# Performance work log

Measured on AMD Instinct MI355X. Metric: run time of the kernel, lower is better.

## Reference

```python
import jax, jax.numpy as jnp
import numpy as np

N_NODES = 50000
N_EDGES = 800000
IN_CH = 128
HID = 32
HEADS = 8
EMB = 64
NEG_SLOPE = 0.2


def _segment_softmax(e, seg, num_segments):
    # e: [E, H] edge scores, seg: [E] destination node ids
    m = jax.ops.segment_max(e, seg, num_segments=num_segments)
    ex = jnp.exp(e - m[seg])
    denom = jax.ops.segment_sum(ex, seg, num_segments=num_segments)
    return ex / (denom[seg] + 1e-16)


def gat_conv(x, src, dst, W, a_src, a_dst, bias, heads, out_ch):
    # x: [N, F_in]; W: [F_in, heads*out_ch]; a_src/a_dst: [heads, out_ch]; bias: [heads*out_ch]
    n = x.shape[0]
    h = (x @ W).reshape(n, heads, out_ch)                 # [N, H, C]
    alpha_src = jnp.sum(h * a_src[None], axis=-1)         # [N, H]
    alpha_dst = jnp.sum(h * a_dst[None], axis=-1)         # [N, H]
    e = jax.nn.leaky_relu(alpha_src[src] + alpha_dst[dst], NEG_SLOPE)  # [E, H]
    alpha = _segment_softmax(e, dst, n)                   # [E, H]
    msg = h[src] * alpha[:, :, None]                      # [E, H, C]
    out = jax.ops.segment_sum(msg, dst, num_segments=n)   # [N, H, C]
    return out.reshape(n, heads * out_ch) + bias


def _with_self_loops(edge_index, n):
    # PyG GATConv default add_self_loops=True
    loop = jnp.arange(n, dtype=edge_index.dtype)
    src = jnp.concatenate([edge_index[0], loop])
    dst = jnp.concatenate([edge_index[1], loop])
    return src, dst


def setup_inputs() -> dict:
    key = jax.random.key(0)
    ks = jax.random.split(key, 16)
    x = jax.random.normal(ks[0], (N_NODES, IN_CH), dtype=jnp.float32)
    edge_index = jax.random.randint(ks[1], (2, N_EDGES), 0, N_NODES, dtype=jnp.int32)

    def glorot(k, shape):
        fan = sum(shape[-2:]) if len(shape) >= 2 else shape[-1]
        return jax.random.normal(k, shape, dtype=jnp.float32) * jnp.sqrt(2.0 / fan)

    # conv1: IN_CH -> HID x HEADS (concat)
    W1 = glorot(ks[2], (IN_CH, HEADS * HID))
    a_src1 = glorot(ks[3], (HEADS, HID))
    a_dst1 = glorot(ks[4], (HEADS, HID))
    b1 = jnp.zeros((HEADS * HID,), jnp.float32)
    # conv2: HID*HEADS -> HID, heads=1
    W2 = glorot(ks[5], (HEADS * HID, HID))
    a_src2 = glorot(ks[6], (1, HID))
    a_dst2 = glorot(ks[7], (1, HID))
    b2 = jnp.zeros((HID,), jnp.float32)
    # conv3: HID -> EMB, heads=1
    W3 = glorot(ks[8], (HID, EMB))
    a_src3 = glorot(ks[9], (1, EMB))
    a_dst3 = glorot(ks[10], (1, EMB))
    b3 = jnp.zeros((EMB,), jnp.float32)
    return {"x": x, "edge_index": edge_index,
            "W1": W1, "a_src1": a_src1, "a_dst1": a_dst1, "b1": b1,
            "W2": W2, "a_src2": a_src2, "a_dst2": a_dst2, "b2": b2,
            "W3": W3, "a_src3": a_src3, "a_dst3": a_dst3, "b3": b3}


def reference(x, edge_index, W1, a_src1, a_dst1, b1, W2, a_src2, a_dst2, b2,
              W3, a_src3, a_dst3, b3):
    src, dst = _with_self_loops(edge_index, x.shape[0])
    h = gat_conv(x, src, dst, W1, a_src1, a_dst1, b1, HEADS, HID)
    h = jax.nn.elu(h)  # dropout is identity in eval mode
    h = gat_conv(h, src, dst, W2, a_src2, a_dst2, b2, 1, HID)
    h = jax.nn.elu(h)
    out = gat_conv(h, src, dst, W3, a_src3, a_dst3, b3, 1, EMB)
    return out
```

## Files before the change

### kernel.cpp

```cpp
#include <hip/hip_runtime.h>
#include <hip/hip_bf16.h>
#include <math.h>

#define N_NODES 50000
#define N_EDGES 800000
#define ET (N_EDGES + N_NODES)
#define F0 128
#define H1 8
#define C1 32
#define D1 (H1*C1)
#define C2 32
#define C3 64
#define CAP 128

typedef unsigned short u16;
typedef unsigned int u32;
typedef __attribute__((ext_vector_type(8))) short short8;
typedef __attribute__((ext_vector_type(4))) float f32x4;

__device__ __forceinline__ float lrelu(float x) { return x >= 0.f ? x : 0.2f * x; }
__device__ __forceinline__ float eluf(float x)  { return x > 0.f ? x : (expf(x) - 1.f); }

__device__ __forceinline__ u16 f2bf(float f) {
    u32 u = __float_as_uint(f);
    return (u16)((u + 0x7FFFu + ((u >> 16) & 1u)) >> 16);
}
__device__ __forceinline__ u32 pack2bf(float lo, float hi) {
    return ((u32)f2bf(hi) << 16) | (u32)f2bf(lo);
}
__device__ __forceinline__ float bf2f(u16 v) {
    return __uint_as_float((u32)v << 16);
}
__device__ __forceinline__ float4 bf4_to_f4(uint2 v) {
    float4 r;
    r.x = __uint_as_float(v.x << 16);
    r.y = __uint_as_float(v.x & 0xFFFF0000u);
    r.z = __uint_as_float(v.y << 16);
    r.w = __uint_as_float(v.y & 0xFFFF0000u);
    return r;
}


__global__ void prep_kernel(const float* __restrict__ W1, const float* __restrict__ W2,
                            const float* __restrict__ W3,
                            u16* __restrict__ W1t, u16* __restrict__ W2t, u16* __restrict__ W3t,
                            int* __restrict__ cnt) {
    int t = blockIdx.x * 256 + threadIdx.x;
    if (t < N_NODES) cnt[t] = 0;
    if (t < F0 * D1) {
        int n = t >> 7, k = t & 127;
        W1t[n * F0 + k] = f2bf(W1[(size_t)k * D1 + n]);
    }
    if (t < D1 * C2) {
        int k = t >> 5, n = t & 31;
        W2t[n * D1 + k] = f2bf(W2[t]);
    }
    if (t < C2 * C3) {
        int k = t >> 6, n = t & 63;
        W3t[n * C2 + k] = f2bf(W3[t]);
    }
}


__global__ void scatterF_kernel(const int* __restrict__ srcArr, const int* __restrict__ dstArr,
                                int* __restrict__ cnt, int* __restrict__ csrF) {
    int e = blockIdx.x * 256 + threadIdx.x;
    if (e >= ET) return;
    int s, d;
    if (e < N_EDGES) { s = srcArr[e]; d = dstArr[e]; } else { s = d = e - N_EDGES; }
    int pos = atomicAdd(&cnt[d], 1);
    csrF[d * CAP + pos] = s;
}


#define WKS 136

__global__ __launch_bounds__(512, 2) void gemm1_mfma(const u16* __restrict__ W1t,
                                                     const float* __restrict__ x,
                                                     const float* __restrict__ aS1,
                                                     const float* __restrict__ aD1,
                                                     u16* __restrict__ h1b,
                                                     float* __restrict__ as,
                                                     float* __restrict__ ad, int M) {
    __shared__ u16 Wt[128][WKS];
    int tid = threadIdx.x;
    int bm = blockIdx.x * 128;

    int w = tid >> 6, lane = tid & 63, l15 = lane & 15, q = lane >> 4;
    int mr = bm + w * 16 + l15;
    if (mr > M - 1) mr = M - 1;

    short8 af[4];
#pragma unroll
    for (int kc = 0; kc < 4; ++kc) {
        const float* ap = x + (size_t)mr * F0 + kc * 32 + q * 8;
        float4 a0 = *(const float4*)ap;
        float4 a1 = *(const float4*)(ap + 4);
        af[kc][0] = (short)f2bf(a0.x); af[kc][1] = (short)f2bf(a0.y);
        af[kc][2] = (short)f2bf(a0.z); af[kc][3] = (short)f2bf(a0.w);
        af[kc][4] = (short)f2bf(a1.x); af[kc][5] = (short)f2bf(a1.y);
        af[kc][6] = (short)f2bf(a1.z); af[kc][7] = (short)f2bf(a1.w);
    }

    f32x4 acc[16];
#pragma unroll
    for (int t = 0; t < 16; ++t) acc[t] = (f32x4){0.f, 0.f, 0.f, 0.f};

#pragma unroll
    for (int half = 0; half < 2; ++half) {
        __syncthreads();
        for (int idx = tid; idx < 128 * F0 / 8; idx += 512) {
            int n = idx >> 4, c = idx & 15;
            *(short8*)&Wt[n][c * 8] =
                *(const short8*)(W1t + (size_t)(half * 128 + n) * F0 + c * 8);
        }
        __syncthreads();
#pragma unroll
        for (int t = 0; t < 8; ++t) {
#pragma unroll
            for (int kc = 0; kc < 4; ++kc) {
                short8 bf = *(const short8*)&Wt[t * 16 + l15][kc * 32 + q * 8];
                acc[half * 8 + t] =
                    __builtin_amdgcn_mfma_f32_16x16x32_bf16(af[kc], bf, acc[half * 8 + t], 0, 0, 0);
            }
        }
    }

#pragma unroll
    for (int r = 0; r < 4; ++r) {
        int row = bm + w * 16 + q * 4 + r;
        if (row >= M) continue;
        size_t base = (size_t)row * D1;
#pragma unroll
        for (int t = 0; t < 16; ++t)
            h1b[base + t * 16 + l15] = f2bf(acc[t][r]);
    }

#pragma unroll
    for (int lh = 0; lh < 8; ++lh) {
        float aS0  = aS1[lh * 32 + l15];
        float aS16 = aS1[lh * 32 + 16 + l15];
        float aD0  = aD1[lh * 32 + l15];
        float aD16 = aD1[lh * 32 + 16 + l15];
#pragma unroll
        for (int r = 0; r < 4; ++r) {
            float s1 = acc[2 * lh][r] * aS0 + acc[2 * lh + 1][r] * aS16;
            float s2 = acc[2 * lh][r] * aD0 + acc[2 * lh + 1][r] * aD16;
            s1 += __shfl_xor(s1, 1); s1 += __shfl_xor(s1, 2);
            s1 += __shfl_xor(s1, 4); s1 += __shfl_xor(s1, 8);
            s2 += __shfl_xor(s2, 1); s2 += __shfl_xor(s2, 2);
            s2 += __shfl_xor(s2, 4); s2 += __shfl_xor(s2, 8);
            int row = bm + w * 16 + q * 4 + r;
            if (l15 == 0 && row < M) {
                as[row * 8 + lh] = s1;
                ad[row * 8 + lh] = s2;
            }
        }
    }
}


__global__ __launch_bounds__(256) void gemm2_mfma(const u16* __restrict__ A,
                                                  const u16* __restrict__ W2t,
                                                  const float* __restrict__ aS2,
                                                  const float* __restrict__ aD2,
                                                  u16* __restrict__ h2b,
                                                  float* __restrict__ as,
                                                  float* __restrict__ ad, int M) {
    int tid = threadIdx.x;
    int bm = blockIdx.x * 64;
    int w = tid >> 6, lane = tid & 63, l15 = lane & 15, q = lane >> 4;
    int mr = bm + w * 16 + l15;
    if (mr > M - 1) mr = M - 1;

    f32x4 acc0 = {0.f, 0.f, 0.f, 0.f};
    f32x4 acc1 = {0.f, 0.f, 0.f, 0.f};
    const u16* b0p = W2t + (size_t)(0 * 16 + l15) * D1;
    const u16* b1p = W2t + (size_t)(1 * 16 + l15) * D1;
#pragma unroll
    for (int k0 = 0; k0 < D1; k0 += 32) {
        short8 af = *(const short8*)(A + (size_t)mr * D1 + k0 + q * 8);
        short8 b0 = *(const short8*)(b0p + k0 + q * 8);
        short8 b1 = *(const short8*)(b1p + k0 + q * 8);
        acc0 = __builtin_amdgcn_mfma_f32_16x16x32_bf16(af, b0, acc0, 0, 0, 0);
        acc1 = __builtin_amdgcn_mfma_f32_16x16x32_bf16(af, b1, acc1, 0, 0, 0);
    }

    float aS0 = aS2[l15], aS16 = aS2[16 + l15];
    float aD0 = aD2[l15], aD16 = aD2[16 + l15];
#pragma unroll
    for (int r = 0; r < 4; ++r) {
        int row = bm + w * 16 + q * 4 + r;
        float s1 = acc0[r] * aS0 + acc1[r] * aS16;
        float s2 = acc0[r] * aD0 + acc1[r] * aD16;
        s1 += __shfl_xor(s1, 1); s1 += __shfl_xor(s1, 2);
        s1 += __shfl_xor(s1, 4); s1 += __shfl_xor(s1, 8);
        s2 += __shfl_xor(s2, 1); s2 += __shfl_xor(s2, 2);
        s2 += __shfl_xor(s2, 4); s2 += __shfl_xor(s2, 8);
        if (row < M) {
            h2b[(size_t)row * C2 + 0 * 16 + l15] = f2bf(acc0[r]);
            h2b[(size_t)row * C2 + 1 * 16 + l15] = f2bf(acc1[r]);
            if (l15 == 0) { as[row] = s1; ad[row] = s2; }
        }
    }
}


__global__ __launch_bounds__(256) void gemm3_mfma(const u16* __restrict__ A,
                                                  const u16* __restrict__ W3t,
                                                  const float* __restrict__ aS3,
                                                  const float* __restrict__ aD3,
                                                  u16* __restrict__ h3b,
                                                  float* __restrict__ as,
                                                  float* __restrict__ ad, int M) {
    int tid = threadIdx.x;
    int bm = blockIdx.x * 64;
    int w = tid >> 6, lane = tid & 63, l15 = lane & 15, q = lane >> 4;
    int mr = bm + w * 16 + l15;
    if (mr > M - 1) mr = M - 1;

    short8 af = *(const short8*)(A + (size_t)mr * C2 + q * 8);

    f32x4 acc[4];
#pragma unroll
    for (int t = 0; t < 4; ++t) {
        short8 bf = *(const short8*)(W3t + (size_t)(t * 16 + l15) * C2 + q * 8);
        f32x4 z = {0.f, 0.f, 0.f, 0.f};
        acc[t] = __builtin_amdgcn_mfma_f32_16x16x32_bf16(af, bf, z, 0, 0, 0);
    }

    float aSv[4], aDv[4];
#pragma unroll
    for (int t = 0; t < 4; ++t) {
        aSv[t] = aS3[t * 16 + l15];
        aDv[t] = aD3[t * 16 + l15];
    }
#pragma unroll
    for (int r = 0; r < 4; ++r) {
        int row = bm + w * 16 + q * 4 + r;
        float s1 = acc[0][r] * aSv[0] + acc[1][r] * aSv[1] + acc[2][r] * aSv[2] + acc[3][r] * aSv[3];
        float s2 = acc[0][r] * aDv[0] + acc[1][r] * aDv[1] + acc[2][r] * aDv[2] + acc[3][r] * aDv[3];
        s1 += __shfl_xor(s1, 1); s1 += __shfl_xor(s1, 2);
        s1 += __shfl_xor(s1, 4); s1 += __shfl_xor(s1, 8);
        s2 += __shfl_xor(s2, 1); s2 += __shfl_xor(s2, 2);
        s2 += __shfl_xor(s2, 4); s2 += __shfl_xor(s2, 8);
        if (row < M) {
            size_t base = (size_t)row * C3;
#pragma unroll
            for (int t = 0; t < 4; ++t)
                h3b[base + t * 16 + l15] = f2bf(acc[t][r]);
            if (l15 == 0) { as[row] = s1; ad[row] = s2; }
        }
    }
}


__global__ __launch_bounds__(256) void agg1_kernel(const int* __restrict__ cnt, const int* __restrict__ csrF,
                                                   const u16* __restrict__ h, const float* __restrict__ as,
                                                   const float* __restrict__ ad, const float* __restrict__ bias,
                                                   u16* __restrict__ outb) {
    int node = blockIdx.x * 4 + (threadIdx.x >> 6);
    if (node >= N_NODES) return;
    int lane = threadIdx.x & 63;
    int hh = lane >> 3;
    int j  = lane & 7;
    int s0 = node * CAP;
    int deg = cnt[node];
    int dmain = deg < 64 ? deg : 64;
    int idxv = (lane < dmain) ? __builtin_nontemporal_load(csrF + s0 + lane) : 0;
    float adw = ad[node * H1 + j];
    const u16* hb = h + hh * C1 + j * 4;

    float4 acc = make_float4(0.f, 0.f, 0.f, 0.f);
    float wsum = 0.f;
    for (int base = 0; base < dmain; base += 8) {
        int sw = __shfl(idxv, base + hh);
        float myw = 0.f;
        if (base + hh < dmain)
            myw = __expf(lrelu(as[sw * H1 + j] + adw));
        wsum += myw;
        int su[8]; uint2 v[8]; float wu[8];
#pragma unroll
        for (int u = 0; u < 8; ++u) su[u] = __shfl(idxv, base + u);
#pragma unroll
        for (int u = 0; u < 8; ++u) v[u] = *(const uint2*)(hb + (size_t)su[u] * D1);
#pragma unroll
        for (int u = 0; u < 8; ++u) wu[u] = __shfl(myw, u * 8 + hh);
#pragma unroll
        for (int u = 0; u < 8; ++u) {
            float4 hv = bf4_to_f4(v[u]);
            acc.x += wu[u] * hv.x;
            acc.y += wu[u] * hv.y;
            acc.z += wu[u] * hv.z;
            acc.w += wu[u] * hv.w;
        }
    }
    float ws = wsum;
    ws += __shfl_xor(ws, 8);
    ws += __shfl_xor(ws, 16);
    ws += __shfl_xor(ws, 32);
    float dsum = __shfl(ws, hh);

    for (int i = 64; i < deg; ++i) {
        int s = csrF[s0 + i];
        float4 hv = bf4_to_f4(*(const uint2*)(hb + (size_t)s * D1));
        float w = __expf(lrelu(as[s * H1 + hh] + ad[node * H1 + hh]));
        dsum += w;
        acc.x += w * hv.x; acc.y += w * hv.y; acc.z += w * hv.z; acc.w += w * hv.w;
    }

    float inv = 1.f / (dsum + 1e-16f);
    int ob = node * D1 + hh * C1 + j * 4;
    const float* bp = bias + hh * C1 + j * 4;
    float rx = eluf(acc.x * inv + bp[0]);
    float ry = eluf(acc.y * inv + bp[1]);
    float rz = eluf(acc.z * inv + bp[2]);
    float rw = eluf(acc.w * inv + bp[3]);
    uint2 pr;
    pr.x = pack2bf(rx, ry);
    pr.y = pack2bf(rz, rw);
    *(uint2*)(outb + ob) = pr;
}


__global__ __launch_bounds__(256) void agg32_kernel(const int* __restrict__ cnt, const int* __restrict__ csrF,
                                                    const u16* __restrict__ h, const float* __restrict__ as,
                                                    const float* __restrict__ ad, const float* __restrict__ bias,
                                                    u16* __restrict__ outb) {
    int node = blockIdx.x * 4 + (threadIdx.x >> 6);
    if (node >= N_NODES) return;
    int lane = threadIdx.x & 63;
    int eg = lane >> 3;
    int cg = lane & 7;
    int s0 = node * CAP;
    int deg = cnt[node];
    int dmain = deg < 64 ? deg : 64;
    int idxv = (lane < dmain) ? __builtin_nontemporal_load(csrF + s0 + lane) : 0;
    float adv = ad[node];

    float wfull = 0.f;
    if (lane < dmain) wfull = __expf(lrelu(as[idxv] + adv));
    float ws = wfull;
#pragma unroll
    for (int o = 1; o < 64; o <<= 1) ws += __shfl_xor(ws, o);
    float dsum = ws;

    float4 acc = make_float4(0.f, 0.f, 0.f, 0.f);
    for (int base = 0; base < dmain; base += 16) {
        int i0 = base + eg;
        int i1 = i0 + 8;
        int sa = __shfl(idxv, i0);
        int sb = __shfl(idxv, i1);
        float wa = __shfl(wfull, i0);
        float wb = __shfl(wfull, i1);
        uint2 va = *(const uint2*)(h + (size_t)sa * C2 + cg * 4);
        uint2 vb = *(const uint2*)(h + (size_t)sb * C2 + cg * 4);
        float4 ha = bf4_to_f4(va);
        float4 hb = bf4_to_f4(vb);
        acc.x += wa * ha.x + wb * hb.x;
        acc.y += wa * ha.y + wb * hb.y;
        acc.z += wa * ha.z + wb * hb.z;
        acc.w += wa * ha.w + wb * hb.w;
    }
    float extra = 0.f;
    for (int i = 64 + eg; i < deg; i += 8) {
        int s = csrF[s0 + i];
        float4 hv = bf4_to_f4(*(const uint2*)(h + (size_t)s * C2 + cg * 4));
        float w = __expf(lrelu(as[s] + adv));
        extra += w;
        acc.x += w * hv.x; acc.y += w * hv.y; acc.z += w * hv.z; acc.w += w * hv.w;
    }
#pragma unroll
    for (int o = 8; o < 64; o <<= 1) {
        acc.x += __shfl_xor(acc.x, o);
        acc.y += __shfl_xor(acc.y, o);
        acc.z += __shfl_xor(acc.z, o);
        acc.w += __shfl_xor(acc.w, o);
        extra += __shfl_xor(extra, o);
    }
    dsum += extra;
    if (eg == 0) {
        float inv = 1.f / (dsum + 1e-16f);
        const float* bp = bias + cg * 4;
        float rx = eluf(acc.x * inv + bp[0]);
        float ry = eluf(acc.y * inv + bp[1]);
        float rz = eluf(acc.z * inv + bp[2]);
        float rw = eluf(acc.w * inv + bp[3]);
        uint2 pr;
        pr.x = pack2bf(rx, ry);
        pr.y = pack2bf(rz, rw);
        *(uint2*)(outb + (size_t)node * C2 + cg * 4) = pr;
    }
}


__global__ __launch_bounds__(256) void agg64_kernel(const int* __restrict__ cnt, const int* __restrict__ csrF,
                                                    const u16* __restrict__ h, const float* __restrict__ as,
                                                    const float* __restrict__ ad, const float* __restrict__ bias,
                                                    float* __restrict__ out) {
    int node = blockIdx.x * 4 + (threadIdx.x >> 6);
    if (node >= N_NODES) return;
    int lane = threadIdx.x & 63;
    int eg = lane >> 4;
    int cg = lane & 15;
    int s0 = node * CAP;
    int deg = cnt[node];
    int dmain = deg < 64 ? deg : 64;
    int idxv = (lane < dmain) ? __builtin_nontemporal_load(csrF + s0 + lane) : 0;
    float adv = ad[node];

    float wfull = 0.f;
    if (lane < dmain) wfull = __expf(lrelu(as[idxv] + adv));
    float ws = wfull;
#pragma unroll
    for (int o = 1; o < 64; o <<= 1) ws += __shfl_xor(ws, o);
    float dsum = ws;

    float4 acc = make_float4(0.f, 0.f, 0.f, 0.f);
    for (int base = 0; base < dmain; base += 8) {
        int i0 = base + eg;
        int i1 = i0 + 4;
        int sa = __shfl(idxv, i0);
        int sb = __shfl(idxv, i1);
        float wa = __shfl(wfull, i0);
        float wb = __shfl(wfull, i1);
        uint2 va = *(const uint2*)(h + (size_t)sa * C3 + cg * 4);
        uint2 vb = *(const uint2*)(h + (size_t)sb * C3 + cg * 4);
        float4 ha = bf4_to_f4(va);
        float4 hb = bf4_to_f4(vb);
        acc.x += wa * ha.x + wb * hb.x;
        acc.y += wa * ha.y + wb * hb.y;
        acc.z += wa * ha.z + wb * hb.z;
        acc.w += wa * ha.w + wb * hb.w;
    }
    float extra = 0.f;
    for (int i = 64 + eg; i < deg; i += 4) {
        int s = csrF[s0 + i];
        float4 hv = bf4_to_f4(*(const uint2*)(h + (size_t)s * C3 + cg * 4));
        float w = __expf(lrelu(as[s] + adv));
        extra += w;
        acc.x += w * hv.x; acc.y += w * hv.y; acc.z += w * hv.z; acc.w += w * hv.w;
    }
#pragma unroll
    for (int o = 16; o < 64; o <<= 1) {
        acc.x += __shfl_xor(acc.x, o);
        acc.y += __shfl_xor(acc.y, o);
        acc.z += __shfl_xor(acc.z, o);
        acc.w += __shfl_xor(acc.w, o);
        extra += __shfl_xor(extra, o);
    }
    dsum += extra;
    if (eg == 0) {
        float inv = 1.f / (dsum + 1e-16f);
        const float* bp = bias + cg * 4;
        float4 r;
        r.x = acc.x * inv + bp[0];
        r.y = acc.y * inv + bp[1];
        r.z = acc.z * inv + bp[2];
        r.w = acc.w * inv + bp[3];
        *(float4*)(out + (size_t)node * C3 + cg * 4) = r;
    }
}


extern "C" void kernel_launch(void* const* d_in, const int* in_sizes, int n_in,
                              void* d_out, int out_size, void* d_ws, size_t ws_size,
                              hipStream_t stream) {
    const float* x   = (const float*)d_in[0];
    const int*   ei  = (const int*)d_in[1];
    const float* W1  = (const float*)d_in[2];
    const float* aS1 = (const float*)d_in[3];
    const float* aD1 = (const float*)d_in[4];
    const float* b1  = (const float*)d_in[5];
    const float* W2  = (const float*)d_in[6];
    const float* aS2 = (const float*)d_in[7];
    const float* aD2 = (const float*)d_in[8];
    const float* b2  = (const float*)d_in[9];
    const float* W3  = (const float*)d_in[10];
    const float* aS3 = (const float*)d_in[11];
    const float* aD3 = (const float*)d_in[12];
    const float* b3  = (const float*)d_in[13];
    float* out = (float*)d_out;

    char* p = (char*)d_ws;
    auto alloc = [&](size_t bytes) -> void* {
        void* r = (void*)p;
        p += (bytes + 255) & ~(size_t)255;
        return r;
    };
    u16*   h1b  = (u16*)alloc((size_t)N_NODES * D1 * 2);
    u16*   x2b  = (u16*)alloc((size_t)N_NODES * D1 * 2);
    u16*   h2b  = (u16*)alloc((size_t)N_NODES * C2 * 2);
    u16*   x3b  = (u16*)alloc((size_t)N_NODES * C2 * 2);
    u16*   h3b  = (u16*)alloc((size_t)N_NODES * C3 * 2);
    int*   cnt  = (int*)alloc((size_t)N_NODES * 4);
    int*   csrF = (int*)alloc((size_t)N_NODES * CAP * 4);
    float* asb  = (float*)alloc((size_t)N_NODES * H1 * 4);
    float* adb  = (float*)alloc((size_t)N_NODES * H1 * 4);
    u16*   W1t  = (u16*)alloc((size_t)F0 * D1 * 2);
    u16*   W2t  = (u16*)alloc((size_t)D1 * C2 * 2);
    u16*   W3t  = (u16*)alloc((size_t)C2 * C3 * 2);

    const int* srcArr = ei;
    const int* dstArr = ei + N_EDGES;

    prep_kernel<<<(N_NODES + 255) / 256, 256, 0, stream>>>(W1, W2, W3, W1t, W2t, W3t, cnt);
    scatterF_kernel<<<(ET + 255) / 256, 256, 0, stream>>>(srcArr, dstArr, cnt, csrF);

    int nb4 = (N_NODES + 3) / 4;
    int mb64 = (N_NODES + 63) / 64;
    int mb128 = (N_NODES + 127) / 128;

    gemm1_mfma<<<mb128, 512, 0, stream>>>(W1t, x, aS1, aD1, h1b, asb, adb, N_NODES);
    agg1_kernel<<<nb4, 256, 0, stream>>>(cnt, csrF, h1b, asb, adb, b1, x2b);

    gemm2_mfma<<<mb64, 256, 0, stream>>>(x2b, W2t, aS2, aD2, h2b, asb, adb, N_NODES);
    agg32_kernel<<<nb4, 256, 0, stream>>>(cnt, csrF, h2b, asb, adb, b2, x3b);

    gemm3_mfma<<<mb64, 256, 0, stream>>>(x3b, W3t, aS3, aD3, h3b, asb, adb, N_NODES);
    agg64_kernel<<<nb4, 256, 0, stream>>>(cnt, csrF, h3b, asb, adb, b3, out);
}
```

Measured before the change: 308.1 us.

## Widen agg1 gathers to 16-byte loads and skip empty edge slots

Layer-1 aggregation now has each lane load 8 bf16 channels with a uint4 load, and the two half-waves handle alternating edges. This replaces eight uint2 loads per lane per 8-edge chunk, and loop iterations past the node's degree are skipped. Layer-2 and layer-3 aggregation guard the second edge load so slots beyond the degree are not fetched, and address math uses 32-bit byte offsets. The CSR scatter uses a nontemporal store. The cost is an extra cross-half shuffle reduction and half the lanes idle on the output write.

```diff
diff --git a/kernel.cpp b/kernel.cpp
--- a/kernel.cpp
+++ b/kernel.cpp
@@ -69,7 +69,7 @@
     int s, d;
     if (e < N_EDGES) { s = srcArr[e]; d = dstArr[e]; } else { s = d = e - N_EDGES; }
     int pos = atomicAdd(&cnt[d], 1);
-    csrF[d * CAP + pos] = s;
+    __builtin_nontemporal_store(s, &csrF[d * CAP + pos]);
 }
 
 
@@ -262,64 +262,105 @@
     int node = blockIdx.x * 4 + (threadIdx.x >> 6);
     if (node >= N_NODES) return;
     int lane = threadIdx.x & 63;
-    int hh = lane >> 3;
-    int j  = lane & 7;
+    int c8 = lane & 31;
+    int pairIdx = lane >> 5;
+    int headW = lane & 7;
+    int slotW = lane >> 3;
+    int hOut = c8 >> 2;
     int s0 = node * CAP;
     int deg = cnt[node];
     int dmain = deg < 64 ? deg : 64;
     int idxv = (lane < dmain) ? __builtin_nontemporal_load(csrF + s0 + lane) : 0;
-    float adw = ad[node * H1 + j];
-    const u16* hb = h + hh * C1 + j * 4;
-
-    float4 acc = make_float4(0.f, 0.f, 0.f, 0.f);
+    float adw = ad[node * H1 + headW];
+    const char* hB = (const char*)h;
+
+    float acc[8];
+#pragma unroll
+    for (int k = 0; k < 8; ++k) acc[k] = 0.f;
     float wsum = 0.f;
+
     for (int base = 0; base < dmain; base += 8) {
-        int sw = __shfl(idxv, base + hh);
+        int sw = __shfl(idxv, base + slotW);
         float myw = 0.f;
-        if (base + hh < dmain)
-            myw = __expf(lrelu(as[sw * H1 + j] + adw));
+        if (base + slotW < dmain)
+            myw = __expf(lrelu(as[sw * H1 + headW] + adw));
         wsum += myw;
-        int su[8]; uint2 v[8]; float wu[8];
-#pragma unroll
-        for (int u = 0; u < 8; ++u) su[u] = __shfl(idxv, base + u);
-#pragma unroll
-        for (int u = 0; u < 8; ++u) v[u] = *(const uint2*)(hb + (size_t)su[u] * D1);
-#pragma unroll
-        for (int u = 0; u < 8; ++u) wu[u] = __shfl(myw, u * 8 + hh);
-#pragma unroll
-        for (int u = 0; u < 8; ++u) {
-            float4 hv = bf4_to_f4(v[u]);
-            acc.x += wu[u] * hv.x;
-            acc.y += wu[u] * hv.y;
-            acc.z += wu[u] * hv.z;
-            acc.w += wu[u] * hv.w;
-        }
-    }
+#pragma unroll
+        for (int u = 0; u < 4; ++u) {
+            if (base + 2 * u >= dmain) break;
+            int e = 2 * u + pairIdx;
+            int s = __shfl(idxv, base + e);
+            float w = __shfl(myw, (e << 3) | hOut);
+            u32 boff = ((u32)s << 9) + (u32)(c8 << 4);
+            uint4 v = *(const uint4*)(hB + boff);
+            float f0 = __uint_as_float(v.x << 16);
+            float f1 = __uint_as_float(v.x & 0xFFFF0000u);
+            float f2 = __uint_as_float(v.y << 16);
+            float f3 = __uint_as_float(v.y & 0xFFFF0000u);
+            float f4 = __uint_as_float(v.z << 16);
+            float f5 = __uint_as_float(v.z & 0xFFFF0000u);
+            float f6 = __uint_as_float(v.w << 16);
+            float f7 = __uint_as_float(v.w & 0xFFFF0000u);
+            acc[0] += w * f0; acc[1] += w * f1;
+            acc[2] += w * f2; acc[3] += w * f3;
+            acc[4] += w * f4; acc[5] += w * f5;
+            acc[6] += w * f6; acc[7] += w * f7;
+        }
+    }
+
     float ws = wsum;
     ws += __shfl_xor(ws, 8);
     ws += __shfl_xor(ws, 16);
     ws += __shfl_xor(ws, 32);
-    float dsum = __shfl(ws, hh);
-
-    for (int i = 64; i < deg; ++i) {
-        int s = csrF[s0 + i];
-        float4 hv = bf4_to_f4(*(const uint2*)(hb + (size_t)s * D1));
-        float w = __expf(lrelu(as[s * H1 + hh] + ad[node * H1 + hh]));
-        dsum += w;
-        acc.x += w * hv.x; acc.y += w * hv.y; acc.z += w * hv.z; acc.w += w * hv.w;
-    }
-
-    float inv = 1.f / (dsum + 1e-16f);
-    int ob = node * D1 + hh * C1 + j * 4;
-    const float* bp = bias + hh * C1 + j * 4;
-    float rx = eluf(acc.x * inv + bp[0]);
-    float ry = eluf(acc.y * inv + bp[1]);
-    float rz = eluf(acc.z * inv + bp[2]);
-    float rw = eluf(acc.w * inv + bp[3]);
-    uint2 pr;
-    pr.x = pack2bf(rx, ry);
-    pr.y = pack2bf(rz, rw);
-    *(uint2*)(outb + ob) = pr;
+    float dsum = __shfl(ws, hOut);
+
+    if (deg > 64) {
+        float adw2 = ad[node * H1 + hOut];
+        for (int i = 64; i < deg; ++i) {
+            int s = csrF[s0 + i];
+            float w = __expf(lrelu(as[s * H1 + hOut] + adw2));
+            u32 boff = ((u32)s << 9) + (u32)(c8 << 4);
+            uint4 v = *(const uint4*)(hB + boff);
+            float wf = pairIdx ? 0.f : w;
+            float f0 = __uint_as_float(v.x << 16);
+            float f1 = __uint_as_float(v.x & 0xFFFF0000u);
+            float f2 = __uint_as_float(v.y << 16);
+            float f3 = __uint_as_float(v.y & 0xFFFF0000u);
+            float f4 = __uint_as_float(v.z << 16);
+            float f5 = __uint_as_float(v.z & 0xFFFF0000u);
+            float f6 = __uint_as_float(v.w << 16);
+            float f7 = __uint_as_float(v.w & 0xFFFF0000u);
+            acc[0] += wf * f0; acc[1] += wf * f1;
+            acc[2] += wf * f2; acc[3] += wf * f3;
+            acc[4] += wf * f4; acc[5] += wf * f5;
+            acc[6] += wf * f6; acc[7] += wf * f7;
+            dsum += w;
+        }
+    }
+
+#pragma unroll
+    for (int k = 0; k < 8; ++k) acc[k] += __shfl_xor(acc[k], 32);
+
+    if (pairIdx == 0) {
+        float inv = 1.f / (dsum + 1e-16f);
+        const float* bp = bias + c8 * 8;
+        float4 b0 = *(const float4*)bp;
+        float4 b1 = *(const float4*)(bp + 4);
+        float r0 = eluf(acc[0] * inv + b0.x);
+        float r1 = eluf(acc[1] * inv + b0.y);
+        float r2 = eluf(acc[2] * inv + b0.z);
+        float r3 = eluf(acc[3] * inv + b0.w);
+        float r4 = eluf(acc[4] * inv + b1.x);
+        float r5 = eluf(acc[5] * inv + b1.y);
+        float r6 = eluf(acc[6] * inv + b1.z);
+        float r7 = eluf(acc[7] * inv + b1.w);
+        uint4 pr;
+        pr.x = pack2bf(r0, r1);
+        pr.y = pack2bf(r2, r3);
+        pr.z = pack2bf(r4, r5);
+        pr.w = pack2bf(r6, r7);
+        *(uint4*)(outb + (size_t)node * D1 + c8 * 8) = pr;
+    }
 }
 
 
@@ -337,6 +378,7 @@
     int dmain = deg < 64 ? deg : 64;
     int idxv = (lane < dmain) ? __builtin_nontemporal_load(csrF + s0 + lane) : 0;
     float adv = ad[node];
+    const char* hB = (const char*)h;
 
     float wfull = 0.f;
     if (lane < dmain) wfull = __expf(lrelu(as[idxv] + adv));
@@ -348,19 +390,21 @@
     float4 acc = make_float4(0.f, 0.f, 0.f, 0.f);
     for (int base = 0; base < dmain; base += 16) {
         int i0 = base + eg;
-        int i1 = i0 + 8;
         int sa = __shfl(idxv, i0);
-        int sb = __shfl(idxv, i1);
         float wa = __shfl(wfull, i0);
-        float wb = __shfl(wfull, i1);
-        uint2 va = *(const uint2*)(h + (size_t)sa * C2 + cg * 4);
-        uint2 vb = *(const uint2*)(h + (size_t)sb * C2 + cg * 4);
+        uint2 va = *(const uint2*)(hB + (((u32)sa << 6) + ((u32)cg << 3)));
         float4 ha = bf4_to_f4(va);
-        float4 hb = bf4_to_f4(vb);
-        acc.x += wa * ha.x + wb * hb.x;
-        acc.y += wa * ha.y + wb * hb.y;
-        acc.z += wa * ha.z + wb * hb.z;
-        acc.w += wa * ha.w + wb * hb.w;
+        acc.x += wa * ha.x; acc.y += wa * ha.y;
+        acc.z += wa * ha.z; acc.w += wa * ha.w;
+        if (base + 8 < dmain) {
+            int i1 = i0 + 8;
+            int sb = __shfl(idxv, i1);
+            float wb = __shfl(wfull, i1);
+            uint2 vb = *(const uint2*)(hB + (((u32)sb << 6) + ((u32)cg << 3)));
+            float4 hb = bf4_to_f4(vb);
+            acc.x += wb * hb.x; acc.y += wb * hb.y;
+            acc.z += wb * hb.z; acc.w += wb * hb.w;
+        }
     }
     float extra = 0.f;
     for (int i = 64 + eg; i < deg; i += 8) {
@@ -408,6 +452,7 @@
     int dmain = deg < 64 ? deg : 64;
     int idxv = (lane < dmain) ? __builtin_nontemporal_load(csrF + s0 + lane) : 0;
     float adv = ad[node];
+    const char* hB = (const char*)h;
 
     float wfull = 0.f;
     if (lane < dmain) wfull = __expf(lrelu(as[idxv] + adv));
@@ -419,19 +464,21 @@
     float4 acc = make_float4(0.f, 0.f, 0.f, 0.f);
     for (int base = 0; base < dmain; base += 8) {
         int i0 = base + eg;
-        int i1 = i0 + 4;
         int sa = __shfl(idxv, i0);
-        int sb = __shfl(idxv, i1);
         float wa = __shfl(wfull, i0);
-        float wb = __shfl(wfull, i1);
-        uint2 va = *(const uint2*)(h + (size_t)sa * C3 + cg * 4);
-        uint2 vb = *(const uint2*)(h + (size_t)sb * C3 + cg * 4);
+        uint2 va = *(const uint2*)(hB + (((u32)sa << 7) + ((u32)cg << 3)));
         float4 ha = bf4_to_f4(va);
-        float4 hb = bf4_to_f4(vb);
-        acc.x += wa * ha.x + wb * hb.x;
-        acc.y += wa * ha.y + wb * hb.y;
-        acc.z += wa * ha.z + wb * hb.z;
-        acc.w += wa * ha.w + wb * hb.w;
+        acc.x += wa * ha.x; acc.y += wa * ha.y;
+        acc.z += wa * ha.z; acc.w += wa * ha.w;
+        if (base + 4 < dmain) {
+            int i1 = i0 + 4;
+            int sb = __shfl(idxv, i1);
+            float wb = __shfl(wfull, i1);
+            uint2 vb = *(const uint2*)(hB + (((u32)sb << 7) + ((u32)cg << 3)));
+            float4 hb = bf4_to_f4(vb);
+            acc.x += wb * hb.x; acc.y += wb * hb.y;
+            acc.z += wb * hb.z; acc.w += wb * hb.w;
+        }
     }
     float extra = 0.f;
     for (int i = 64 + eg; i < deg; i += 4) {
```

Result: slower. 328.7 us (+6.7%).
